# Kernel optimization log

Hardware: AMD Instinct MI355X
Metric: run time of the kernel (lower is better)

The kernel has to match this reference:

```python
import jax, jax.numpy as jnp
import numpy as np

T = 4
TAU = 2.0
THR = 0.2
N_NODES = 50000
N_EDGES = 400000
N_LINKS = 50000
N_FEAT = 256
ENC0, ENC1 = 256, 128
DEC = 64


def _make_spike(grad_fn):
    @jax.custom_vjp
    def spike(v):
        return (v >= 0).astype(v.dtype)

    def fwd(v):
        return (v >= 0).astype(v.dtype), v

    def bwd(res, g):
        return (g * grad_fn(res),)

    spike.defvjp(fwd, bwd)
    return spike


def _sg_sigmoid(x, alpha=4.0):
    s = jax.nn.sigmoid(alpha * x)
    return alpha * s * (1.0 - s)


def _sg_pwl(x, w=0.5, c=0.0):
    return jnp.where(jnp.abs(x) < w, 1.0 / w, c)


spike_sig = _make_spike(_sg_sigmoid)   # default LIFNode surrogate (Sigmoid, alpha=4)
spike_pwl = _make_spike(_sg_pwl)       # PiecewiseLeakyReLU(w=0.5, c=0.0)


def _lif(v, x, spike_fn):
    # decay_input=False, v_reset=None -> soft reset, decay toward 0
    v = v * (1.0 - 1.0 / TAU) + x
    s = spike_fn(v - THR)
    return v - s * THR, s


def setup_inputs() -> dict:
    key = jax.random.key(0)
    ks = jax.random.split(key, 12)
    x = jax.random.uniform(ks[0], (N_NODES, N_FEAT), jnp.float32)
    edge_src = jax.random.randint(ks[1], (N_EDGES,), 0, N_NODES, jnp.int32)
    edge_dst = jax.random.randint(ks[2], (N_EDGES,), 0, N_NODES, jnp.int32)
    edge_w = jax.random.uniform(ks[3], (N_EDGES,), jnp.float32)
    nodes_s = jax.random.randint(ks[4], (N_LINKS,), 0, N_NODES, jnp.int32)
    nodes_t = jax.random.randint(ks[5], (N_LINKS,), 0, N_NODES, jnp.int32)
    W1 = jax.random.normal(ks[6], (N_FEAT, ENC0), jnp.float32) / np.sqrt(N_FEAT)
    W2 = jax.random.normal(ks[7], (N_FEAT + ENC0, ENC1), jnp.float32) / np.sqrt(N_FEAT + ENC0)
    Wd = jax.random.normal(ks[8], (ENC1, DEC), jnp.float32) / np.sqrt(ENC1)
    bd = jax.random.normal(ks[9], (DEC,), jnp.float32) * 0.01
    w_rec = jax.random.normal(ks[10], (DEC,), jnp.float32)
    return {"x": x, "W1": W1, "W2": W2, "Wd": Wd, "bd": bd, "w_rec": w_rec,
            "edge_w": edge_w, "edge_src": edge_src, "edge_dst": edge_dst,
            "nodes_s": nodes_s, "nodes_t": nodes_t}


def reference(x, W1, W2, Wd, bd, w_rec, edge_w, edge_src, edge_dst, nodes_s, nodes_t):
    N = x.shape[0]
    L = nodes_s.shape[0]
    key = jax.random.key(42)
    ew = edge_w[:, None]

    def propagate(feat):  # sparse adj @ feat via edge-list scatter-add
        return jax.ops.segment_sum(feat[edge_src] * ew, edge_dst, num_segments=N)

    def poisson(v, k):  # PoissonEncoder: spike ~ Bernoulli(v), zero gradient
        u = jax.random.uniform(k, v.shape, v.dtype)
        return (u <= jax.lax.stop_gradient(v)).astype(v.dtype)

    carry0 = (jnp.zeros((N, ENC0), x.dtype),              # v of layer0 z-LIF
              jnp.zeros((N, N_FEAT + ENC0), x.dtype),      # v of layer1 h-LIF
              jnp.zeros((N, ENC1), x.dtype),               # v of layer1 z-LIF
              jnp.zeros((2 * L, DEC), x.dtype))            # v of decoder LIF

    def step(carry, t):
        v0z, v1h, v1z, vdec = carry
        kt = jax.random.fold_in(key, t)
        k1, k2 = jax.random.split(kt)
        inp = poisson(x, k1)                    # inputs_encoding(x)
        h0 = propagate(inp)                     # layer0 GraphConvolution
        hs0 = poisson(h0, k2)                   # layer0 PoissonEncoder
        v0z, zs0 = _lif(v0z, hs0 @ W1, spike_pwl)
        inp1 = jnp.concatenate([zs0, hs0], axis=1)  # [N, 512]
        h1 = propagate(inp1)                    # layer1 GraphConvolution
        v1h, hs1 = _lif(v1h, h1, spike_sig)     # layer1 LIFNode (default surrogate)
        v1z, zs1 = _lif(v1z, hs1 @ W2, spike_pwl)
        hcat = jnp.concatenate([zs1[nodes_s], zs1[nodes_t]], axis=0)  # [2L, 128]
        vdec, zd = _lif(vdec, hcat @ Wd + bd, spike_pwl)
        y_t = jnp.sum(zd[:L] * w_rec * zd[L:], axis=1)  # WeightedInnerProduct_Link
        return (v0z, v1h, v1z, vdec), y_t

    _, y = jax.lax.scan(step, carry0, jnp.arange(T))  # y: [T, L]
    return jax.nn.sigmoid(jnp.mean(y, axis=0))        # PotentialOutput readout + sigmoid
```

## Files before the change

kernel.cpp:

```cpp
#include <hip/hip_runtime.h>
#include <stdint.h>
#include <math.h>

#define NN    50000
#define NE    400000
#define NL    50000
#define TOT   12800000

#define JAX_PARTITIONABLE 1

struct K8 { uint32_t a[4]; uint32_t b[4]; };

__host__ __device__ inline uint32_t rotl32(uint32_t x, int r){ return (x<<r)|(x>>(32-r)); }

__host__ __device__ inline void tf2x32(uint32_t k0, uint32_t k1, uint32_t x0, uint32_t x1,
                                       uint32_t &o0, uint32_t &o1) {
  uint32_t k2 = k0 ^ k1 ^ 0x1BD11BDAu;
  x0 += k0; x1 += k1;
#define TFR(r) { x0 += x1; x1 = rotl32(x1,(r)); x1 ^= x0; }
  TFR(13) TFR(15) TFR(26) TFR(6)
  x0 += k1; x1 += k2 + 1u;
  TFR(17) TFR(29) TFR(16) TFR(24)
  x0 += k2; x1 += k0 + 2u;
  TFR(13) TFR(15) TFR(26) TFR(6)
  x0 += k0; x1 += k1 + 3u;
  TFR(17) TFR(29) TFR(16) TFR(24)
  x0 += k1; x1 += k2 + 4u;
  TFR(13) TFR(15) TFR(26) TFR(6)
  x0 += k2; x1 += k0 + 5u;
#undef TFR
  o0 = x0; o1 = x1;
}

__device__ inline float u01(uint32_t b){
  return __uint_as_float((b>>9) | 0x3f800000u) - 1.0f;
}

__device__ inline uint32_t jax_bits32(uint32_t ka, uint32_t kb, uint32_t i, uint32_t total){
#if JAX_PARTITIONABLE
  uint32_t o0,o1; tf2x32(ka,kb, 0u, i, o0,o1); return o0^o1;
#else
  uint32_t h = total>>1; uint32_t o0,o1;
  if (i < h){ tf2x32(ka,kb, i, i+h, o0,o1); return o0; }
  else      { tf2x32(ka,kb, i-h, i, o0,o1); return o1; }
#endif
}

__device__ inline double shflxor_d(double x, int m){
  union { double d; int i[2]; } u; u.d = x;
  u.i[0] = __shfl_xor(u.i[0], m, 64);
  u.i[1] = __shfl_xor(u.i[1], m, 64);
  return u.d;
}

__device__ inline bool lif32(float &v, float a){
  v = __fadd_rn(__fmul_rn(v, 0.5f), a);
  float d = __fsub_rn(v, 0.2f);
  bool s = (d >= 0.0f);
  v = s ? d : v;
  return s;
}

#define FORCE_V(x) asm volatile("" : "+v"(x))

__device__ inline float bitmaskf(uint32_t w, int b, float wr){
#if __has_builtin(__builtin_amdgcn_sbfe)
  int m = __builtin_amdgcn_sbfe((int)w, b, 1);
#else
  int m = ((int)(w << (31-b))) >> 31;
#endif
  return __int_as_float(__float_as_int(wr) & m);
}

__global__ __launch_bounds__(256) void k_hist(const int* __restrict__ dst, int* __restrict__ cnt){
  int e = blockIdx.x*256 + threadIdx.x;
  if (e < NE) atomicAdd(&cnt[dst[e]], 1);
}

__global__ __launch_bounds__(1024) void k_scan(const int* __restrict__ cnt,
    int* __restrict__ rp, int* __restrict__ cur){
  __shared__ int buf[1024];
  __shared__ int carry;
  int tid = threadIdx.x;
  if (tid==0) carry = 0;
  __syncthreads();
  for (int base=0; base<NN; base+=1024){
    int v = (base+tid < NN) ? cnt[base+tid] : 0;
    buf[tid] = v; __syncthreads();
    for (int off=1; off<1024; off<<=1){
      int t = (tid>=off) ? buf[tid-off] : 0;
      __syncthreads();
      buf[tid] += t;
      __syncthreads();
    }
    int excl = buf[tid] - v + carry;
    if (base+tid < NN){ rp[base+tid] = excl; cur[base+tid] = excl; }
    __syncthreads();
    if (tid==0) carry += buf[1023];
    __syncthreads();
  }
  if (tid==0) rp[NN] = NE;
}

__global__ __launch_bounds__(256) void k_scatter(const int* __restrict__ dst,
    int* __restrict__ cur, int* __restrict__ eidx){
  int e = blockIdx.x*256 + threadIdx.x;
  if (e < NE){ int p = atomicAdd(&cur[dst[e]], 1); eidx[p] = e; }
}

__global__ __launch_bounds__(256) void k_sortrow(const int* __restrict__ rp,
    int* __restrict__ eidx, const int* __restrict__ esrc, const float* __restrict__ ew,
    int* __restrict__ csrc, float* __restrict__ cw){
  int n = blockIdx.x*256 + threadIdx.x;
  if (n >= NN) return;
  int lo = rp[n], hi = rp[n+1];
  for (int a=lo+1; a<hi; a++){
    int k = eidx[a]; int b = a-1;
    while (b>=lo && eidx[b]>k){ eidx[b+1]=eidx[b]; b--; }
    eidx[b+1] = k;
  }
  for (int p=lo; p<hi; p++){ int e = eidx[p]; csrc[p] = esrc[e]; cw[p] = ew[e]; }
}


__global__ __launch_bounds__(256) void k_pois_x(const float* __restrict__ x,
    uint64_t* __restrict__ bits, K8 K){
  int n = blockIdx.x, f = threadIdx.x;
  uint32_t i = (uint32_t)n*256u + (uint32_t)f;
  float xv = x[i];
  uint64_t pack[4];
  #pragma unroll
  for (int t=0;t<4;t++){
    bool b = (u01(jax_bits32(K.a[t],K.b[t], i, TOT)) <= xv);
    pack[t] = __ballot(b);
  }
  if ((f & 63)==0){
    uint64_t* dst = bits + ((size_t)n*4 + (f>>6))*4;
    #pragma unroll
    for (int t=0;t<4;t++) dst[t] = pack[t];
  }
}

__global__ __launch_bounds__(256) void k_h0(const int* __restrict__ rp,
    const int* __restrict__ csrc, const float* __restrict__ cw,
    const uint64_t* __restrict__ inb, uint64_t* __restrict__ outb, K8 K){
  int n = blockIdx.x, f = threadIdx.x;
  int wi = f>>6, sh = f&63;
  int lo = rp[n], hi = rp[n+1];
  float a[4] = {0.f,0.f,0.f,0.f};
  for (int p=lo;p<hi;p++){
    int s = csrc[p]; float w = cw[p];
    const uint64_t* bp = inb + ((size_t)s*4 + wi)*4;
    uint64_t w0=bp[0], w1=bp[1], w2=bp[2], w3=bp[3];
    a[0] = __fadd_rn(a[0], ((w0>>sh)&1ull) ? w : 0.0f);
    a[1] = __fadd_rn(a[1], ((w1>>sh)&1ull) ? w : 0.0f);
    a[2] = __fadd_rn(a[2], ((w2>>sh)&1ull) ? w : 0.0f);
    a[3] = __fadd_rn(a[3], ((w3>>sh)&1ull) ? w : 0.0f);
  }
  uint32_t i = (uint32_t)n*256u + (uint32_t)f;
  uint64_t pack[4];
  #pragma unroll
  for (int t=0;t<4;t++){
    bool b = (u01(jax_bits32(K.a[t],K.b[t], i, TOT)) <= a[t]);
    pack[t] = __ballot(b);
  }
  if (sh==0){
    uint64_t* dst = outb + ((size_t)n*4 + wi)*4;
    #pragma unroll
    for (int t=0;t<4;t++) dst[t] = pack[t];
  }
}

__global__ __launch_bounds__(256) void k_z0(const uint64_t* __restrict__ inb,
    const float* __restrict__ W, uint64_t* __restrict__ outb){
  __shared__ __align__(16) float sp[8*64*4];
  int tid = threadIdx.x;
  int wave = tid>>6, lane = tid&63;
  int g = wave>>1;
  int ch = wave&1;
  int colBase = ch*128;
  int n0 = blockIdx.x*8;
  float acc[4][4][2];
  #pragma unroll
  for (int t=0;t<4;t++)
    #pragma unroll
    for (int i=0;i<4;i++){ acc[t][i][0]=0.0f; acc[t][i][1]=0.0f; }

  for (int kt=0; kt<4; kt++){
    #pragma unroll
    for (int rep=0; rep<2; rep++){
      int idx = rep*256 + tid;
      int i = idx>>6, k = idx&63;
      const uint64_t* bp = inb + (((size_t)(n0+i))*4 + kt)*4;
      uint64_t w0=bp[0], w1=bp[1], w2=bp[2], w3=bp[3];
      float4 f;
      f.x = ((w0>>k)&1ull) ? 1.0f : 0.0f;
      f.y = ((w1>>k)&1ull) ? 1.0f : 0.0f;
      f.z = ((w2>>k)&1ull) ? 1.0f : 0.0f;
      f.w = ((w3>>k)&1ull) ? 1.0f : 0.0f;
      *(float4*)&sp[(i*64+k)*4] = f;
    }
    __syncthreads();
    const float* Wrow = W + (size_t)(kt*64)*256 + colBase + lane;
    #pragma unroll 4
    for (int q=0;q<64;q++){
      float wr0 = Wrow[(size_t)q*256];
      float wr1 = Wrow[(size_t)q*256 + 64];
      float4 s0 = *(const float4*)&sp[((g*4+0)*64+q)*4];
      float4 s1 = *(const float4*)&sp[((g*4+1)*64+q)*4];
      float4 s2 = *(const float4*)&sp[((g*4+2)*64+q)*4];
      float4 s3 = *(const float4*)&sp[((g*4+3)*64+q)*4];
      acc[0][0][0]=__fmaf_rn(s0.x,wr0,acc[0][0][0]); acc[0][0][1]=__fmaf_rn(s0.x,wr1,acc[0][0][1]);
      acc[1][0][0]=__fmaf_rn(s0.y,wr0,acc[1][0][0]); acc[1][0][1]=__fmaf_rn(s0.y,wr1,acc[1][0][1]);
      acc[2][0][0]=__fmaf_rn(s0.z,wr0,acc[2][0][0]); acc[2][0][1]=__fmaf_rn(s0.z,wr1,acc[2][0][1]);
      acc[3][0][0]=__fmaf_rn(s0.w,wr0,acc[3][0][0]); acc[3][0][1]=__fmaf_rn(s0.w,wr1,acc[3][0][1]);
      acc[0][1][0]=__fmaf_rn(s1.x,wr0,acc[0][1][0]); acc[0][1][1]=__fmaf_rn(s1.x,wr1,acc[0][1][1]);
      acc[1][1][0]=__fmaf_rn(s1.y,wr0,acc[1][1][0]); acc[1][1][1]=__fmaf_rn(s1.y,wr1,acc[1][1][1]);
      acc[2][1][0]=__fmaf_rn(s1.z,wr0,acc[2][1][0]); acc[2][1][1]=__fmaf_rn(s1.z,wr1,acc[2][1][1]);
      acc[3][1][0]=__fmaf_rn(s1.w,wr0,acc[3][1][0]); acc[3][1][1]=__fmaf_rn(s1.w,wr1,acc[3][1][1]);
      acc[0][2][0]=__fmaf_rn(s2.x,wr0,acc[0][2][0]); acc[0][2][1]=__fmaf_rn(s2.x,wr1,acc[0][2][1]);
      acc[1][2][0]=__fmaf_rn(s2.y,wr0,acc[1][2][0]); acc[1][2][1]=__fmaf_rn(s2.y,wr1,acc[1][2][1]);
      acc[2][2][0]=__fmaf_rn(s2.z,wr0,acc[2][2][0]); acc[2][2][1]=__fmaf_rn(s2.z,wr1,acc[2][2][1]);
      acc[3][2][0]=__fmaf_rn(s2.w,wr0,acc[3][2][0]); acc[3][2][1]=__fmaf_rn(s2.w,wr1,acc[3][2][1]);
      acc[0][3][0]=__fmaf_rn(s3.x,wr0,acc[0][3][0]); acc[0][3][1]=__fmaf_rn(s3.x,wr1,acc[0][3][1]);
      acc[1][3][0]=__fmaf_rn(s3.y,wr0,acc[1][3][0]); acc[1][3][1]=__fmaf_rn(s3.y,wr1,acc[1][3][1]);
      acc[2][3][0]=__fmaf_rn(s3.z,wr0,acc[2][3][0]); acc[2][3][1]=__fmaf_rn(s3.z,wr1,acc[2][3][1]);
      acc[3][3][0]=__fmaf_rn(s3.w,wr0,acc[3][3][0]); acc[3][3][1]=__fmaf_rn(s3.w,wr1,acc[3][3][1]);
    }
    __syncthreads();
  }

  #pragma unroll
  for (int i=0;i<4;i++){
    int node = n0 + g*4 + i;
    float v0 = 0.0f, v1 = 0.0f;
    uint64_t p0[4], p1[4];
    #pragma unroll
    for (int t=0;t<4;t++){
      bool s0 = lif32(v0, acc[t][i][0]);
      bool s1 = lif32(v1, acc[t][i][1]);
      p0[t] = __ballot(s0);
      p1[t] = __ballot(s1);
    }
    if (lane==0){
      uint64_t* d0 = outb + ((size_t)node*4 + ch*2    )*4;
      uint64_t* d1 = outb + ((size_t)node*4 + ch*2 + 1)*4;
      #pragma unroll
      for (int t=0;t<4;t++){ d0[t]=p0[t]; d1[t]=p1[t]; }
    }
  }
}

__global__ __launch_bounds__(512) void k_h1(const int* __restrict__ rp,
    const int* __restrict__ csrc, const float* __restrict__ cw,
    const uint64_t* __restrict__ zs0b, const uint64_t* __restrict__ hs0b,
    uint64_t* __restrict__ hs1b){
  int n = blockIdx.x, f = threadIdx.x;
  int wi = f>>6, sh = f&63;
  const uint64_t* plane = (wi<4) ? zs0b : hs0b;
  int wo = wi & 3;
  int lo = rp[n], hi = rp[n+1];
  float a[4] = {0.f,0.f,0.f,0.f};
  for (int p=lo;p<hi;p++){
    int s = csrc[p]; float w = cw[p];
    const uint64_t* bp = plane + ((size_t)s*4 + wo)*4;
    uint64_t w0=bp[0], w1=bp[1], w2=bp[2], w3=bp[3];
    a[0] = __fadd_rn(a[0], ((w0>>sh)&1ull) ? w : 0.0f);
    a[1] = __fadd_rn(a[1], ((w1>>sh)&1ull) ? w : 0.0f);
    a[2] = __fadd_rn(a[2], ((w2>>sh)&1ull) ? w : 0.0f);
    a[3] = __fadd_rn(a[3], ((w3>>sh)&1ull) ? w : 0.0f);
  }
  float v = 0.0f;
  uint64_t pack[4];
  #pragma unroll
  for (int t=0;t<4;t++){
    bool s = lif32(v, a[t]);
    pack[t] = __ballot(s);
  }
  if (sh==0){
    uint64_t* dst = hs1b + ((size_t)n*8 + wi)*4;
    #pragma unroll
    for (int t=0;t<4;t++) dst[t] = pack[t];
  }
}

__global__ __launch_bounds__(128) void k_z1(const uint64_t* __restrict__ inb,
    const float* __restrict__ W, uint64_t* __restrict__ outb){
  __shared__ __align__(16) float sp[8*64*4];
  int tid = threadIdx.x;
  int g = tid>>6, lane = tid&63;
  int n0 = blockIdx.x*8;
  float acc[4][4][2];
  #pragma unroll
  for (int t=0;t<4;t++)
    #pragma unroll
    for (int i=0;i<4;i++){ acc[t][i][0]=0.0f; acc[t][i][1]=0.0f; }

  for (int kt=0; kt<8; kt++){
    #pragma unroll
    for (int rep=0; rep<4; rep++){
      int idx = rep*128 + tid;
      int i = idx>>6, k = idx&63;
      const uint64_t* bp = inb + (((size_t)(n0+i))*8 + kt)*4;
      uint64_t w0=bp[0], w1=bp[1], w2=bp[2], w3=bp[3];
      float4 f;
      f.x = ((w0>>k)&1ull) ? 1.0f : 0.0f;
      f.y = ((w1>>k)&1ull) ? 1.0f : 0.0f;
      f.z = ((w2>>k)&1ull) ? 1.0f : 0.0f;
      f.w = ((w3>>k)&1ull) ? 1.0f : 0.0f;
      *(float4*)&sp[(i*64+k)*4] = f;
    }
    __syncthreads();
    const float* Wrow = W + (size_t)(kt*64)*128 + lane;
    #pragma unroll 4
    for (int q=0;q<64;q++){
      float wr0 = Wrow[(size_t)q*128];
      float wr1 = Wrow[(size_t)q*128 + 64];
      float4 s0 = *(const float4*)&sp[((g*4+0)*64+q)*4];
      float4 s1 = *(const float4*)&sp[((g*4+1)*64+q)*4];
      float4 s2 = *(const float4*)&sp[((g*4+2)*64+q)*4];
      float4 s3 = *(const float4*)&sp[((g*4+3)*64+q)*4];
      acc[0][0][0]=__fmaf_rn(s0.x,wr0,acc[0][0][0]); acc[0][0][1]=__fmaf_rn(s0.x,wr1,acc[0][0][1]);
      acc[1][0][0]=__fmaf_rn(s0.y,wr0,acc[1][0][0]); acc[1][0][1]=__fmaf_rn(s0.y,wr1,acc[1][0][1]);
      acc[2][0][0]=__fmaf_rn(s0.z,wr0,acc[2][0][0]); acc[2][0][1]=__fmaf_rn(s0.z,wr1,acc[2][0][1]);
      acc[3][0][0]=__fmaf_rn(s0.w,wr0,acc[3][0][0]); acc[3][0][1]=__fmaf_rn(s0.w,wr1,acc[3][0][1]);
      acc[0][1][0]=__fmaf_rn(s1.x,wr0,acc[0][1][0]); acc[0][1][1]=__fmaf_rn(s1.x,wr1,acc[0][1][1]);
      acc[1][1][0]=__fmaf_rn(s1.y,wr0,acc[1][1][0]); acc[1][1][1]=__fmaf_rn(s1.y,wr1,acc[1][1][1]);
      acc[2][1][0]=__fmaf_rn(s1.z,wr0,acc[2][1][0]); acc[2][1][1]=__fmaf_rn(s1.z,wr1,acc[2][1][1]);
      acc[3][1][0]=__fmaf_rn(s1.w,wr0,acc[3][1][0]); acc[3][1][1]=__fmaf_rn(s1.w,wr1,acc[3][1][1]);
      acc[0][2][0]=__fmaf_rn(s2.x,wr0,acc[0][2][0]); acc[0][2][1]=__fmaf_rn(s2.x,wr1,acc[0][2][1]);
      acc[1][2][0]=__fmaf_rn(s2.y,wr0,acc[1][2][0]); acc[1][2][1]=__fmaf_rn(s2.y,wr1,acc[1][2][1]);
      acc[2][2][0]=__fmaf_rn(s2.z,wr0,acc[2][2][0]); acc[2][2][1]=__fmaf_rn(s2.z,wr1,acc[2][2][1]);
      acc[3][2][0]=__fmaf_rn(s2.w,wr0,acc[3][2][0]); acc[3][2][1]=__fmaf_rn(s2.w,wr1,acc[3][2][1]);
      acc[0][3][0]=__fmaf_rn(s3.x,wr0,acc[0][3][0]); acc[0][3][1]=__fmaf_rn(s3.x,wr1,acc[0][3][1]);
      acc[1][3][0]=__fmaf_rn(s3.y,wr0,acc[1][3][0]); acc[1][3][1]=__fmaf_rn(s3.y,wr1,acc[1][3][1]);
      acc[2][3][0]=__fmaf_rn(s3.z,wr0,acc[2][3][0]); acc[2][3][1]=__fmaf_rn(s3.z,wr1,acc[2][3][1]);
      acc[3][3][0]=__fmaf_rn(s3.w,wr0,acc[3][3][0]); acc[3][3][1]=__fmaf_rn(s3.w,wr1,acc[3][3][1]);
    }
    __syncthreads();
  }

  #pragma unroll
  for (int i=0;i<4;i++){
    int node = n0 + g*4 + i;
    float v0 = 0.0f, v1 = 0.0f;
    uint64_t p0[4], p1[4];
    #pragma unroll
    for (int t=0;t<4;t++){
      bool s0 = lif32(v0, acc[t][i][0]);
      bool s1 = lif32(v1, acc[t][i][1]);
      p0[t] = __ballot(s0);
      p1[t] = __ballot(s1);
    }
    if (lane==0){
      uint64_t* d0 = outb + ((size_t)node*2 + 0)*4;
      uint64_t* d1 = outb + ((size_t)node*2 + 1)*4;
      #pragma unroll
      for (int t=0;t<4;t++){ d0[t]=p0[t]; d1[t]=p1[t]; }
    }
  }
}

__global__ __launch_bounds__(128) void k_dec_y(const int* __restrict__ ns,
    const int* __restrict__ nt, const uint64_t* __restrict__ zs1b,
    const float* __restrict__ Wd, const float* __restrict__ bd,
    const float* __restrict__ wrec, float* __restrict__ out){
  int i = blockIdx.x;
  int tid = threadIdx.x;
  int row = tid>>6, j = tid&63;
  int node = row ? nt[i] : ns[i];
  float bdj = bd[j];
  double wrecj = (double)wrec[j];
  __shared__ uint64_t sw[2];

  uint32_t wlo[2][4], whi[2][4];
  const uint64_t* bp = zs1b + (size_t)node*8;
  #pragma unroll
  for (int g=0;g<2;g++)
    #pragma unroll
    for (int t=0;t<4;t++){
      uint64_t w8 = bp[g*4+t];
      wlo[g][t] = (uint32_t)w8;
      whi[g][t] = (uint32_t)(w8>>32);
      FORCE_V(wlo[g][t]); FORCE_V(whi[g][t]);
    }

  float acc[4] = {0.f,0.f,0.f,0.f};
  #pragma unroll
  for (int g=0;g<2;g++){
    #pragma unroll
    for (int h=0;h<2;h++){
      #pragma unroll
      for (int c=0;c<2;c++){
        float wr[16];
        #pragma unroll
        for (int q=0;q<16;q++) wr[q] = Wd[(size_t)(g*64+h*32+c*16+q)*64 + j];
        #pragma unroll
        for (int q=0;q<16;q++){
          int b = c*16+q;
          #pragma unroll
          for (int t=0;t<4;t++){
            uint32_t wv = h ? whi[g][t] : wlo[g][t];
            acc[t] = __fadd_rn(acc[t], bitmaskf(wv, b, wr[q]));
          }
        }
      }
    }
  }

  float v = 0.0f;
  double ysum = 0.0;
  #pragma unroll
  for (int t=0;t<4;t++){
    float a = __fadd_rn(acc[t], bdj);
    bool s = lif32(v, a);
    uint64_t bw = __ballot(s);
    if (j==0) sw[row] = bw;
    __syncthreads();
    uint64_t m = sw[0] & sw[1];
    __syncthreads();
    double term = ((m>>j)&1ull) ? wrecj : 0.0;
    #pragma unroll
    for (int off=1; off<64; off<<=1) term += shflxor_d(term, off);
    ysum += term;
  }
  if (tid==0) out[i] = (float)(1.0/(1.0 + exp(-0.25*ysum)));
}

extern "C" void kernel_launch(void* const* d_in, const int* in_sizes, int n_in,
                              void* d_out, int out_size, void* d_ws, size_t ws_size,
                              hipStream_t stream) {
  const float* x    = (const float*)d_in[0];
  const float* W1   = (const float*)d_in[1];
  const float* W2   = (const float*)d_in[2];
  const float* Wd   = (const float*)d_in[3];
  const float* bd   = (const float*)d_in[4];
  const float* wrec = (const float*)d_in[5];
  const float* ew   = (const float*)d_in[6];
  const int* esrc   = (const int*)d_in[7];
  const int* edst   = (const int*)d_in[8];
  const int* ns     = (const int*)d_in[9];
  const int* nt     = (const int*)d_in[10];
  float* out = (float*)d_out;
  (void)in_sizes; (void)n_in; (void)out_size; (void)ws_size;

  char* p = (char*)d_ws;
  uint64_t* inpb = (uint64_t*)p; p += (size_t)NN*16*8;
  uint64_t* hs0b = (uint64_t*)p; p += (size_t)NN*16*8;
  uint64_t* zs0b = (uint64_t*)p; p += (size_t)NN*16*8;
  uint64_t* hs1b = (uint64_t*)p; p += (size_t)NN*32*8;
  uint64_t* zs1b = (uint64_t*)p; p += (size_t)NN*8*8;
  int*   eidx = (int*)p;   p += (size_t)NE*4;
  int*   csrc = (int*)p;   p += (size_t)NE*4;
  float* cw   = (float*)p; p += (size_t)NE*4;
  int*   cnt  = (int*)p;   p += (size_t)(NN+2)*4;
  int*   rp   = (int*)p;   p += (size_t)(NN+2)*4;
  int*   cur  = (int*)p;   p += (size_t)(NN+2)*4;

  K8 K1, K2;
  for (int t=0;t<4;t++){
    uint32_t kt0,kt1;
    tf2x32(0u, 42u, 0u, (uint32_t)t, kt0, kt1);
#if JAX_PARTITIONABLE
    tf2x32(kt0, kt1, 0u, 0u, K1.a[t], K1.b[t]);
    tf2x32(kt0, kt1, 0u, 1u, K2.a[t], K2.b[t]);
#else
    uint32_t A0,B0,A1,B1;
    tf2x32(kt0, kt1, 0u, 2u, A0, B0);
    tf2x32(kt0, kt1, 1u, 3u, A1, B1);
    K1.a[t]=A0; K1.b[t]=A1; K2.a[t]=B0; K2.b[t]=B1;
#endif
  }

  hipMemsetAsync(cnt, 0, (size_t)NN*4, stream);
  k_hist   <<<(NE+255)/256, 256, 0, stream>>>(edst, cnt);
  k_scan   <<<1, 1024, 0, stream>>>(cnt, rp, cur);
  k_scatter<<<(NE+255)/256, 256, 0, stream>>>(edst, cur, eidx);
  k_sortrow<<<(NN+255)/256, 256, 0, stream>>>(rp, eidx, esrc, ew, csrc, cw);

  k_pois_x<<<NN, 256, 0, stream>>>(x, inpb, K1);
  k_h0    <<<NN, 256, 0, stream>>>(rp, csrc, cw, inpb, hs0b, K2);
  k_z0    <<<NN/8, 256, 0, stream>>>(hs0b, W1, zs0b);
  k_h1    <<<NN, 512, 0, stream>>>(rp, csrc, cw, zs0b, hs0b, hs1b);
  k_z1    <<<NN/8, 128, 0, stream>>>(hs1b, W2, zs1b);
  k_dec_y <<<NL, 128, 0, stream>>>(ns, nt, zs1b, Wd, bd, wrec, out);
}
```

Measured before the change: 1.633 ms.

## Enlarge register tiles in spike GEMMs and use wave-shuffle prefix scan

The two spike-matrix GEMM kernels (z0, z1) now cover 16 nodes per block instead of 8, and each thread holds a 4x4x4 accumulator tile over four output columns instead of two. This reuses each shared-memory spike load across more FMAs and halves the block count. The cost is higher register pressure, which the launch bounds of 2 try to cap, and more complex output packing in z1 where each half-wave handles 32 columns. Separately, the single-block CSR prefix scan replaces a shared-memory Hillis-Steele scan with wave shuffles, cutting the number of barriers.

Result: faster. 1.588 ms (-2.8%).

```diff
diff --git a/kernel.cpp b/kernel.cpp
--- a/kernel.cpp
+++ b/kernel.cpp
@@ -79,24 +79,35 @@
 
 __global__ __launch_bounds__(1024) void k_scan(const int* __restrict__ cnt,
     int* __restrict__ rp, int* __restrict__ cur){
-  __shared__ int buf[1024];
-  __shared__ int carry;
+  __shared__ int ws[16];
+  __shared__ int wp[17];
   int tid = threadIdx.x;
-  if (tid==0) carry = 0;
-  __syncthreads();
+  int lane = tid & 63, wid = tid >> 6;
+  int carry = 0;
   for (int base=0; base<NN; base+=1024){
     int v = (base+tid < NN) ? cnt[base+tid] : 0;
-    buf[tid] = v; __syncthreads();
-    for (int off=1; off<1024; off<<=1){
-      int t = (tid>=off) ? buf[tid-off] : 0;
-      __syncthreads();
-      buf[tid] += t;
-      __syncthreads();
-    }
-    int excl = buf[tid] - v + carry;
+    int x = v;
+    #pragma unroll
+    for (int off=1; off<64; off<<=1){
+      int u = __shfl_up(x, off, 64);
+      if (lane >= off) x += u;
+    }
+    if (lane==63) ws[wid] = x;
+    __syncthreads();
+    if (wid==0){
+      int s = (lane<16) ? ws[lane] : 0;
+      #pragma unroll
+      for (int off=1; off<16; off<<=1){
+        int u = __shfl_up(s, off, 64);
+        if (lane >= off) s += u;
+      }
+      if (lane<16) wp[lane+1] = s;
+      if (lane==0) wp[0] = 0;
+    }
+    __syncthreads();
+    int excl = x - v + wp[wid] + carry;
     if (base+tid < NN){ rp[base+tid] = excl; cur[base+tid] = excl; }
-    __syncthreads();
-    if (tid==0) carry += buf[1023];
+    carry += wp[16];
     __syncthreads();
   }
   if (tid==0) rp[NN] = NE;
@@ -171,24 +182,23 @@
   }
 }
 
-__global__ __launch_bounds__(256) void k_z0(const uint64_t* __restrict__ inb,
+__global__ __launch_bounds__(256, 2) void k_z0(const uint64_t* __restrict__ inb,
     const float* __restrict__ W, uint64_t* __restrict__ outb){
-  __shared__ __align__(16) float sp[8*64*4];
+  __shared__ __align__(16) float sp[16*64*4];
   int tid = threadIdx.x;
-  int wave = tid>>6, lane = tid&63;
-  int g = wave>>1;
-  int ch = wave&1;
-  int colBase = ch*128;
-  int n0 = blockIdx.x*8;
-  float acc[4][4][2];
+  int g = tid>>6, lane = tid&63;
+  int n0 = blockIdx.x*16;
+  float acc[4][4][4];
   #pragma unroll
   for (int t=0;t<4;t++)
     #pragma unroll
-    for (int i=0;i<4;i++){ acc[t][i][0]=0.0f; acc[t][i][1]=0.0f; }
+    for (int i=0;i<4;i++)
+      #pragma unroll
+      for (int c=0;c<4;c++) acc[t][i][c]=0.0f;
 
   for (int kt=0; kt<4; kt++){
     #pragma unroll
-    for (int rep=0; rep<2; rep++){
+    for (int rep=0; rep<4; rep++){
       int idx = rep*256 + tid;
       int i = idx>>6, k = idx&63;
       const uint64_t* bp = inb + (((size_t)(n0+i))*4 + kt)*4;
@@ -201,31 +211,26 @@
       *(float4*)&sp[(i*64+k)*4] = f;
     }
     __syncthreads();
-    const float* Wrow = W + (size_t)(kt*64)*256 + colBase + lane;
+    const float* Wrow = W + (size_t)(kt*64)*256 + lane;
     #pragma unroll 4
     for (int q=0;q<64;q++){
-      float wr0 = Wrow[(size_t)q*256];
-      float wr1 = Wrow[(size_t)q*256 + 64];
+      const float* wb = Wrow + (size_t)q*256;
+      float wr0 = wb[0], wr1 = wb[64], wr2 = wb[128], wr3 = wb[192];
       float4 s0 = *(const float4*)&sp[((g*4+0)*64+q)*4];
       float4 s1 = *(const float4*)&sp[((g*4+1)*64+q)*4];
       float4 s2 = *(const float4*)&sp[((g*4+2)*64+q)*4];
       float4 s3 = *(const float4*)&sp[((g*4+3)*64+q)*4];
-      acc[0][0][0]=__fmaf_rn(s0.x,wr0,acc[0][0][0]); acc[0][0][1]=__fmaf_rn(s0.x,wr1,acc[0][0][1]);
-      acc[1][0][0]=__fmaf_rn(s0.y,wr0,acc[1][0][0]); acc[1][0][1]=__fmaf_rn(s0.y,wr1,acc[1][0][1]);
-      acc[2][0][0]=__fmaf_rn(s0.z,wr0,acc[2][0][0]); acc[2][0][1]=__fmaf_rn(s0.z,wr1,acc[2][0][1]);
-      acc[3][0][0]=__fmaf_rn(s0.w,wr0,acc[3][0][0]); acc[3][0][1]=__fmaf_rn(s0.w,wr1,acc[3][0][1]);
-      acc[0][1][0]=__fmaf_rn(s1.x,wr0,acc[0][1][0]); acc[0][1][1]=__fmaf_rn(s1.x,wr1,acc[0][1][1]);
-      acc[1][1][0]=__fmaf_rn(s1.y,wr0,acc[1][1][0]); acc[1][1][1]=__fmaf_rn(s1.y,wr1,acc[1][1][1]);
-      acc[2][1][0]=__fmaf_rn(s1.z,wr0,acc[2][1][0]); acc[2][1][1]=__fmaf_rn(s1.z,wr1,acc[2][1][1]);
-      acc[3][1][0]=__fmaf_rn(s1.w,wr0,acc[3][1][0]); acc[3][1][1]=__fmaf_rn(s1.w,wr1,acc[3][1][1]);
-      acc[0][2][0]=__fmaf_rn(s2.x,wr0,acc[0][2][0]); acc[0][2][1]=__fmaf_rn(s2.x,wr1,acc[0][2][1]);
-      acc[1][2][0]=__fmaf_rn(s2.y,wr0,acc[1][2][0]); acc[1][2][1]=__fmaf_rn(s2.y,wr1,acc[1][2][1]);
-      acc[2][2][0]=__fmaf_rn(s2.z,wr0,acc[2][2][0]); acc[2][2][1]=__fmaf_rn(s2.z,wr1,acc[2][2][1]);
-      acc[3][2][0]=__fmaf_rn(s2.w,wr0,acc[3][2][0]); acc[3][2][1]=__fmaf_rn(s2.w,wr1,acc[3][2][1]);
-      acc[0][3][0]=__fmaf_rn(s3.x,wr0,acc[0][3][0]); acc[0][3][1]=__fmaf_rn(s3.x,wr1,acc[0][3][1]);
-      acc[1][3][0]=__fmaf_rn(s3.y,wr0,acc[1][3][0]); acc[1][3][1]=__fmaf_rn(s3.y,wr1,acc[1][3][1]);
-      acc[2][3][0]=__fmaf_rn(s3.z,wr0,acc[2][3][0]); acc[2][3][1]=__fmaf_rn(s3.z,wr1,acc[2][3][1]);
-      acc[3][3][0]=__fmaf_rn(s3.w,wr0,acc[3][3][0]); acc[3][3][1]=__fmaf_rn(s3.w,wr1,acc[3][3][1]);
+      #define FMA4(ti, sv) \
+        acc[ti][0][0]=__fmaf_rn(s0.sv,wr0,acc[ti][0][0]); acc[ti][0][1]=__fmaf_rn(s0.sv,wr1,acc[ti][0][1]); \
+        acc[ti][0][2]=__fmaf_rn(s0.sv,wr2,acc[ti][0][2]); acc[ti][0][3]=__fmaf_rn(s0.sv,wr3,acc[ti][0][3]); \
+        acc[ti][1][0]=__fmaf_rn(s1.sv,wr0,acc[ti][1][0]); acc[ti][1][1]=__fmaf_rn(s1.sv,wr1,acc[ti][1][1]); \
+        acc[ti][1][2]=__fmaf_rn(s1.sv,wr2,acc[ti][1][2]); acc[ti][1][3]=__fmaf_rn(s1.sv,wr3,acc[ti][1][3]); \
+        acc[ti][2][0]=__fmaf_rn(s2.sv,wr0,acc[ti][2][0]); acc[ti][2][1]=__fmaf_rn(s2.sv,wr1,acc[ti][2][1]); \
+        acc[ti][2][2]=__fmaf_rn(s2.sv,wr2,acc[ti][2][2]); acc[ti][2][3]=__fmaf_rn(s2.sv,wr3,acc[ti][2][3]); \
+        acc[ti][3][0]=__fmaf_rn(s3.sv,wr0,acc[ti][3][0]); acc[ti][3][1]=__fmaf_rn(s3.sv,wr1,acc[ti][3][1]); \
+        acc[ti][3][2]=__fmaf_rn(s3.sv,wr2,acc[ti][3][2]); acc[ti][3][3]=__fmaf_rn(s3.sv,wr3,acc[ti][3][3]);
+      FMA4(0, x) FMA4(1, y) FMA4(2, z) FMA4(3, w)
+      #undef FMA4
     }
     __syncthreads();
   }
@@ -233,20 +238,19 @@
   #pragma unroll
   for (int i=0;i<4;i++){
     int node = n0 + g*4 + i;
-    float v0 = 0.0f, v1 = 0.0f;
-    uint64_t p0[4], p1[4];
+    float v[4] = {0.f,0.f,0.f,0.f};
     #pragma unroll
     for (int t=0;t<4;t++){
-      bool s0 = lif32(v0, acc[t][i][0]);
-      bool s1 = lif32(v1, acc[t][i][1]);
-      p0[t] = __ballot(s0);
-      p1[t] = __ballot(s1);
-    }
-    if (lane==0){
-      uint64_t* d0 = outb + ((size_t)node*4 + ch*2    )*4;
-      uint64_t* d1 = outb + ((size_t)node*4 + ch*2 + 1)*4;
+      uint64_t b[4];
       #pragma unroll
-      for (int t=0;t<4;t++){ d0[t]=p0[t]; d1[t]=p1[t]; }
+      for (int c=0;c<4;c++){
+        bool s = lif32(v[c], acc[t][i][c]);
+        b[c] = __ballot(s);
+      }
+      if (lane==0){
+        #pragma unroll
+        for (int c=0;c<4;c++) outb[((size_t)node*4 + c)*4 + t] = b[c];
+      }
     }
   }
 }
@@ -284,21 +288,25 @@
   }
 }
 
-__global__ __launch_bounds__(128) void k_z1(const uint64_t* __restrict__ inb,
+__global__ __launch_bounds__(128, 2) void k_z1(const uint64_t* __restrict__ inb,
     const float* __restrict__ W, uint64_t* __restrict__ outb){
-  __shared__ __align__(16) float sp[8*64*4];
+  __shared__ __align__(16) float sp[16*64*4];
   int tid = threadIdx.x;
-  int g = tid>>6, lane = tid&63;
-  int n0 = blockIdx.x*8;
-  float acc[4][4][2];
+  int wv = tid>>6, lane = tid&63;
+  int half = lane>>5, cl = lane&31;
+  int gi = wv*2 + half;
+  int n0 = blockIdx.x*16;
+  float acc[4][4][4];
   #pragma unroll
   for (int t=0;t<4;t++)
     #pragma unroll
-    for (int i=0;i<4;i++){ acc[t][i][0]=0.0f; acc[t][i][1]=0.0f; }
+    for (int i=0;i<4;i++)
+      #pragma unroll
+      for (int c=0;c<4;c++) acc[t][i][c]=0.0f;
 
   for (int kt=0; kt<8; kt++){
     #pragma unroll
-    for (int rep=0; rep<4; rep++){
+    for (int rep=0; rep<8; rep++){
       int idx = rep*128 + tid;
       int i = idx>>6, k = idx&63;
       const uint64_t* bp = inb + (((size_t)(n0+i))*8 + kt)*4;
@@ -311,52 +319,53 @@
       *(float4*)&sp[(i*64+k)*4] = f;
     }
     __syncthreads();
-    const float* Wrow = W + (size_t)(kt*64)*128 + lane;
+    const float* Wrow = W + (size_t)(kt*64)*128 + cl;
     #pragma unroll 4
     for (int q=0;q<64;q++){
-      float wr0 = Wrow[(size_t)q*128];
-      float wr1 = Wrow[(size_t)q*128 + 64];
-      float4 s0 = *(const float4*)&sp[((g*4+0)*64+q)*4];
-      float4 s1 = *(const float4*)&sp[((g*4+1)*64+q)*4];
-      float4 s2 = *(const float4*)&sp[((g*4+2)*64+q)*4];
-      float4 s3 = *(const float4*)&sp[((g*4+3)*64+q)*4];
-      acc[0][0][0]=__fmaf_rn(s0.x,wr0,acc[0][0][0]); acc[0][0][1]=__fmaf_rn(s0.x,wr1,acc[0][0][1]);
-      acc[1][0][0]=__fmaf_rn(s0.y,wr0,acc[1][0][0]); acc[1][0][1]=__fmaf_rn(s0.y,wr1,acc[1][0][1]);
-      acc[2][0][0]=__fmaf_rn(s0.z,wr0,acc[2][0][0]); acc[2][0][1]=__fmaf_rn(s0.z,wr1,acc[2][0][1]);
-      acc[3][0][0]=__fmaf_rn(s0.w,wr0,acc[3][0][0]); acc[3][0][1]=__fmaf_rn(s0.w,wr1,acc[3][0][1]);
-      acc[0][1][0]=__fmaf_rn(s1.x,wr0,acc[0][1][0]); acc[0][1][1]=__fmaf_rn(s1.x,wr1,acc[0][1][1]);
-      acc[1][1][0]=__fmaf_rn(s1.y,wr0,acc[1][1][0]); acc[1][1][1]=__fmaf_rn(s1.y,wr1,acc[1][1][1]);
-      acc[2][1][0]=__fmaf_rn(s1.z,wr0,acc[2][1][0]); acc[2][1][1]=__fmaf_rn(s1.z,wr1,acc[2][1][1]);
-      acc[3][1][0]=__fmaf_rn(s1.w,wr0,acc[3][1][0]); acc[3][1][1]=__fmaf_rn(s1.w,wr1,acc[3][1][1]);
-      acc[0][2][0]=__fmaf_rn(s2.x,wr0,acc[0][2][0]); acc[0][2][1]=__fmaf_rn(s2.x,wr1,acc[0][2][1]);
-      acc[1][2][0]=__fmaf_rn(s2.y,wr0,acc[1][2][0]); acc[1][2][1]=__fmaf_rn(s2.y,wr1,acc[1][2][1]);
-      acc[2][2][0]=__fmaf_rn(s2.z,wr0,acc[2][2][0]); acc[2][2][1]=__fmaf_rn(s2.z,wr1,acc[2][2][1]);
-      acc[3][2][0]=__fmaf_rn(s2.w,wr0,acc[3][2][0]); acc[3][2][1]=__fmaf_rn(s2.w,wr1,acc[3][2][1]);
-      acc[0][3][0]=__fmaf_rn(s3.x,wr0,acc[0][3][0]); acc[0][3][1]=__fmaf_rn(s3.x,wr1,acc[0][3][1]);
-      acc[1][3][0]=__fmaf_rn(s3.y,wr0,acc[1][3][0]); acc[1][3][1]=__fmaf_rn(s3.y,wr1,acc[1][3][1]);
-      acc[2][3][0]=__fmaf_rn(s3.z,wr0,acc[2][3][0]); acc[2][3][1]=__fmaf_rn(s3.z,wr1,acc[2][3][1]);
-      acc[3][3][0]=__fmaf_rn(s3.w,wr0,acc[3][3][0]); acc[3][3][1]=__fmaf_rn(s3.w,wr1,acc[3][3][1]);
+      const float* wb = Wrow + (size_t)q*128;
+      float wr0 = wb[0], wr1 = wb[32], wr2 = wb[64], wr3 = wb[96];
+      float4 s0 = *(const float4*)&sp[((gi*4+0)*64+q)*4];
+      float4 s1 = *(const float4*)&sp[((gi*4+1)*64+q)*4];
+      float4 s2 = *(const float4*)&sp[((gi*4+2)*64+q)*4];
+      float4 s3 = *(const float4*)&sp[((gi*4+3)*64+q)*4];
+      #define FMA4(ti, sv) \
+        acc[ti][0][0]=__fmaf_rn(s0.sv,wr0,acc[ti][0][0]); acc[ti][0][1]=__fmaf_rn(s0.sv,wr1,acc[ti][0][1]); \
+        acc[ti][0][2]=__fmaf_rn(s0.sv,wr2,acc[ti][0][2]); acc[ti][0][3]=__fmaf_rn(s0.sv,wr3,acc[ti][0][3]); \
+        acc[ti][1][0]=__fmaf_rn(s1.sv,wr0,acc[ti][1][0]); acc[ti][1][1]=__fmaf_rn(s1.sv,wr1,acc[ti][1][1]); \
+        acc[ti][1][2]=__fmaf_rn(s1.sv,wr2,acc[ti][1][2]); acc[ti][1][3]=__fmaf_rn(s1.sv,wr3,acc[ti][1][3]); \
+        acc[ti][2][0]=__fmaf_rn(s2.sv,wr0,acc[ti][2][0]); acc[ti][2][1]=__fmaf_rn(s2.sv,wr1,acc[ti][2][1]); \
+        acc[ti][2][2]=__fmaf_rn(s2.sv,wr2,acc[ti][2][2]); acc[ti][2][3]=__fmaf_rn(s2.sv,wr3,acc[ti][2][3]); \
+        acc[ti][3][0]=__fmaf_rn(s3.sv,wr0,acc[ti][3][0]); acc[ti][3][1]=__fmaf_rn(s3.sv,wr1,acc[ti][3][1]); \
+        acc[ti][3][2]=__fmaf_rn(s3.sv,wr2,acc[ti][3][2]); acc[ti][3][3]=__fmaf_rn(s3.sv,wr3,acc[ti][3][3]);
+      FMA4(0, x) FMA4(1, y) FMA4(2, z) FMA4(3, w)
+      #undef FMA4
     }
     __syncthreads();
   }
 
   #pragma unroll
   for (int i=0;i<4;i++){
-    int node = n0 + g*4 + i;
-    float v0 = 0.0f, v1 = 0.0f;
-    uint64_t p0[4], p1[4];
+    int node = n0 + gi*4 + i;
+    float v[4] = {0.f,0.f,0.f,0.f};
     #pragma unroll
     for (int t=0;t<4;t++){
-      bool s0 = lif32(v0, acc[t][i][0]);
-      bool s1 = lif32(v1, acc[t][i][1]);
-      p0[t] = __ballot(s0);
-      p1[t] = __ballot(s1);
-    }
-    if (lane==0){
-      uint64_t* d0 = outb + ((size_t)node*2 + 0)*4;
-      uint64_t* d1 = outb + ((size_t)node*2 + 1)*4;
-      #pragma unroll
-      for (int t=0;t<4;t++){ d0[t]=p0[t]; d1[t]=p1[t]; }
+      uint64_t b0,b1,b2,b3;
+      { bool s = lif32(v[0], acc[t][i][0]); b0 = __ballot(s); }
+      { bool s = lif32(v[1], acc[t][i][1]); b1 = __ballot(s); }
+      { bool s = lif32(v[2], acc[t][i][2]); b2 = __ballot(s); }
+      { bool s = lif32(v[3], acc[t][i][3]); b3 = __ballot(s); }
+      if (cl==0){
+        uint64_t m0, m1;
+        if (half==0){
+          m0 = (b0 & 0xffffffffull) | ((b1 & 0xffffffffull)<<32);
+          m1 = (b2 & 0xffffffffull) | ((b3 & 0xffffffffull)<<32);
+        } else {
+          m0 = (b0>>32) | ((b1>>32)<<32);
+          m1 = (b2>>32) | ((b3>>32)<<32);
+        }
+        outb[((size_t)node*2 + 0)*4 + t] = m0;
+        outb[((size_t)node*2 + 1)*4 + t] = m1;
+      }
     }
   }
 }
@@ -480,8 +489,8 @@
 
   k_pois_x<<<NN, 256, 0, stream>>>(x, inpb, K1);
   k_h0    <<<NN, 256, 0, stream>>>(rp, csrc, cw, inpb, hs0b, K2);
-  k_z0    <<<NN/8, 256, 0, stream>>>(hs0b, W1, zs0b);
+  k_z0    <<<NN/16, 256, 0, stream>>>(hs0b, W1, zs0b);
   k_h1    <<<NN, 512, 0, stream>>>(rp, csrc, cw, zs0b, hs0b, hs1b);
-  k_z1    <<<NN/8, 128, 0, stream>>>(hs1b, W2, zs1b);
+  k_z1    <<<NN/16, 128, 0, stream>>>(hs1b, W2, zs1b);
   k_dec_y <<<NL, 128, 0, stream>>>(ns, nt, zs1b, Wd, bd, wrec, out);
 }
```
